# Performance work log

Hardware: AMD Instinct MI355X
Metric: run time of the kernel (lower is better)

## Reference

```python
import jax, jax.numpy as jnp
import numpy as np

N_ENTITY = 64368
N_REL = 40
DIM = 128
NUM_BASES = 8
N_EDGES = 1_200_000
BATCH = 64
MAX_SEED = 32


def setup_inputs() -> dict:
    key = jax.random.key(0)
    ks = jax.random.split(key, 12)
    basis = jax.random.normal(ks[0], (NUM_BASES, N_ENTITY, DIM), jnp.float32) * 0.02
    att = jax.random.normal(ks[1], (N_REL, NUM_BASES), jnp.float32) * 0.1
    root = jax.random.normal(ks[2], (N_ENTITY, DIM), jnp.float32) * 0.02
    rgcn_bias = jnp.zeros((DIM,), jnp.float32)
    xav = 1.414 / np.sqrt(DIM)  # xavier_uniform gain=1.414 scale
    attn_a = jax.random.uniform(ks[3], (DIM, DIM), jnp.float32, -xav, xav)
    attn_b = jax.random.uniform(ks[4], (DIM, 1), jnp.float32, -xav, xav)
    output_bias = jnp.zeros((N_ENTITY,), jnp.float32)
    edge_index = jax.random.randint(ks[5], (2, N_EDGES), 0, N_ENTITY, jnp.int32)
    edge_type = jax.random.randint(ks[6], (N_EDGES,), 0, N_REL, jnp.int32)
    lengths = jax.random.randint(ks[7], (BATCH,), 1, MAX_SEED + 1, jnp.int32)
    seed_mask = jnp.arange(MAX_SEED)[None, :] < lengths[:, None]  # ragged seed sets
    seed_idx = jax.random.randint(ks[8], (BATCH, MAX_SEED), 0, N_ENTITY, jnp.int32)
    labels = jax.random.randint(ks[9], (BATCH,), 0, N_ENTITY, jnp.int32)
    return dict(basis=basis, att=att, root=root, rgcn_bias=rgcn_bias,
                attn_a=attn_a, attn_b=attn_b, output_bias=output_bias,
                edge_index=edge_index, edge_type=edge_type,
                seed_idx=seed_idx, seed_mask=seed_mask, labels=labels)


def reference(basis, att, root, rgcn_bias, attn_a, attn_b, output_bias,
              edge_index, edge_type, seed_idx, seed_mask, labels):
    # ---- RGCNConv with x=None (old PyG): msg_e = (att[rel_e] @ basis)[src_e] ----
    src, dst = edge_index[0], edge_index[1]
    coeff = att[edge_type]                      # [E, B]
    # loop over small fixed num_bases to avoid materializing [B, E, D]
    msg = coeff[:, 0:1] * basis[0][src]         # [E, D]
    for b in range(1, basis.shape[0]):
        msg = msg + coeff[:, b:b + 1] * basis[b][src]
    agg = jax.ops.segment_sum(msg, dst, num_segments=root.shape[0])  # scatter-add
    nodes = agg + root + rgcn_bias              # [N, D] node features

    # ---- per-seed-set gather + self-attention pooling ----
    h = nodes[seed_idx]                         # [Bt, L, D]
    e = jnp.squeeze(jnp.tanh(h @ attn_a) @ attn_b, -1)  # [Bt, L]
    e = jnp.where(seed_mask, e, -jnp.inf)
    attn = jax.nn.softmax(e, axis=-1)
    u = jnp.einsum('bl,bld->bd', attn, h)       # [Bt, D] user reps

    # ---- scores = F.linear(u, nodes, output.bias); CE loss ----
    scores = u @ nodes.T + output_bias          # [Bt, N]
    logp = jax.nn.log_softmax(scores, axis=-1)
    loss = -jnp.mean(jnp.take_along_axis(logp, labels[:, None].astype(jnp.int32), axis=1))
    return scores, loss
```

## Files before the change

kernel.cpp:

```cpp
#include <hip/hip_runtime.h>
#include <hip/hip_bf16.h>

#define N_ENT 64368
#define DIM 128
#define NB 8
#define NREL 40
#define BATCH 64
#define MAXSEED 32
#define OPAD 16

__device__ __forceinline__ unsigned pack_bf2(float x, float y) {
    union { float f; unsigned u; } a, b;
    a.f = x; b.f = y;
    unsigned ra = a.u + 0x7FFFu + ((a.u >> 16) & 1u);
    unsigned rb = b.u + 0x7FFFu + ((b.u >> 16) & 1u);
    return (ra >> 16) | (rb & 0xFFFF0000u);
}

__global__ void mask_norm_kernel(const unsigned char* __restrict__ raw,
                                 int* __restrict__ outMask) {
    __shared__ int s_ni, s_nf;
    int t = threadIdx.x;
    if (t == 0) { s_ni = 0; s_nf = 0; }
    __syncthreads();
    const unsigned int* u32 = (const unsigned int*)raw;
    int not_int = 0, not_flt = 0;
    for (int i = t; i < 512; i += blockDim.x) {
        unsigned int g = u32[i];
        if (g != 0u && g != 1u) not_int = 1;
        if (g != 0u && g != 0x3F800000u) not_flt = 1;
    }
    if (not_int) atomicOr(&s_ni, 1);
    if (not_flt) atomicOr(&s_nf, 1);
    __syncthreads();
    int mode = (!s_ni) ? 0 : ((!s_nf) ? 1 : 2);
    for (int i = t; i < BATCH * MAXSEED; i += blockDim.x) {
        int v;
        if (mode == 0)      v = ((const int*)raw)[i] != 0;
        else if (mode == 1) v = (((const float*)raw)[i] != 0.0f);
        else                v = raw[i] != 0;
        outMask[i] = v;
    }
}

__global__ __launch_bounds__(256) void hist_kernel(
    const int* __restrict__ eidx, int E,
    int* __restrict__ cntS, int* __restrict__ cntD)
{
    const int t = blockIdx.x * blockDim.x + threadIdx.x;
    const int e0 = t * 4;
    if (((E & 3) == 0) && e0 + 3 < E) {
        int4 s4 = *(const int4*)(eidx + e0);
        int4 d4 = *(const int4*)(eidx + E + e0);
        atomicAdd(&cntS[s4.x], 1); atomicAdd(&cntS[s4.y], 1);
        atomicAdd(&cntS[s4.z], 1); atomicAdd(&cntS[s4.w], 1);
        atomicAdd(&cntD[d4.x], 1); atomicAdd(&cntD[d4.y], 1);
        atomicAdd(&cntD[d4.z], 1); atomicAdd(&cntD[d4.w], 1);
    } else {
        for (int e = e0; e < E && e < e0 + 4; ++e) {
            atomicAdd(&cntS[eidx[e]], 1);
            atomicAdd(&cntD[eidx[e + E]], 1);
        }
    }
}

__global__ __launch_bounds__(1024) void scan2_kernel(
    const int* __restrict__ cntS, int* __restrict__ rpS, int* __restrict__ ofS,
    const int* __restrict__ cntD, int* __restrict__ rpD, int* __restrict__ ofD)
{
    const int* cnt = blockIdx.x ? cntD : cntS;
    int* row_ptr   = blockIdx.x ? rpD : rpS;
    int* ofs       = blockIdx.x ? ofD : ofS;
    __shared__ int s[1024];
    const int t = threadIdx.x;
    const int CH = 63;
    const int base = t * CH;
    int sum = 0;
    for (int j = 0; j < CH; ++j) { int p = base + j; if (p < N_ENT) sum += cnt[p]; }
    s[t] = sum;
    for (int off = 1; off < 1024; off <<= 1) {
        __syncthreads();
        int x = (t >= off) ? s[t - off] : 0;
        __syncthreads();
        s[t] += x;
    }
    __syncthreads();
    int run = s[t] - sum;
    for (int j = 0; j < CH; ++j) {
        int p = base + j;
        if (p < N_ENT) { row_ptr[p] = run; ofs[(size_t)p * OPAD] = run; run += cnt[p]; }
    }
    if (t == 1023) row_ptr[N_ENT] = s[1023];
}

__global__ __launch_bounds__(256) void scatS_kernel(
    const int* __restrict__ eidx, const int* __restrict__ etype, int E,
    int* __restrict__ ofsS, unsigned* __restrict__ srcSorted)
{
    const int t = blockIdx.x * blockDim.x + threadIdx.x;
    const int e0 = t * 4;
    if (((E & 3) == 0) && e0 + 3 < E) {
        int4 s4 = *(const int4*)(eidx + e0);
        int4 d4 = *(const int4*)(eidx + E + e0);
        int4 r4 = *(const int4*)(etype + e0);
        int p0 = atomicAdd(&ofsS[(size_t)s4.x * OPAD], 1);
        int p1 = atomicAdd(&ofsS[(size_t)s4.y * OPAD], 1);
        int p2 = atomicAdd(&ofsS[(size_t)s4.z * OPAD], 1);
        int p3 = atomicAdd(&ofsS[(size_t)s4.w * OPAD], 1);
        srcSorted[p0] = ((unsigned)d4.x << 6) | (unsigned)r4.x;
        srcSorted[p1] = ((unsigned)d4.y << 6) | (unsigned)r4.y;
        srcSorted[p2] = ((unsigned)d4.z << 6) | (unsigned)r4.z;
        srcSorted[p3] = ((unsigned)d4.w << 6) | (unsigned)r4.w;
    } else {
        for (int e = e0; e < E && e < e0 + 4; ++e) {
            int p = atomicAdd(&ofsS[(size_t)eidx[e] * OPAD], 1);
            srcSorted[p] = ((unsigned)eidx[e + E] << 6) | (unsigned)etype[e];
        }
    }
}

__global__ __launch_bounds__(256) void msg_kernel(
    const float* __restrict__ basis, const float* __restrict__ att,
    const int* __restrict__ row_ptrS, const unsigned* __restrict__ srcSorted,
    int* __restrict__ ofsD, unsigned* __restrict__ msg)
{
    __shared__ float att_s[NREL * NB];
    const int t = threadIdx.x;
    for (int i = t; i < NREL * NB; i += 256) att_s[i] = att[i];
    __syncthreads();
    const int lane = t & 63;
    const int s = blockIdx.x * 4 + (t >> 6);
    const int r0 = row_ptrS[s], r1 = row_ptrS[s + 1];
    if (r0 == r1) return;
    float2 B[NB];
#pragma unroll
    for (int b = 0; b < NB; ++b)
        B[b] = ((const float2*)(basis + ((size_t)b * N_ENT + s) * DIM))[lane];
    for (int i = r0; i < r1; i += 4) {
        const int m = min(4, r1 - i);
        unsigned pk_l = (lane < m) ? srcSorted[i + lane] : 0u;
        int q_l = 0;
        if (lane < m) q_l = atomicAdd(&ofsD[(size_t)(pk_l >> 6) * OPAD], 1);
        for (int j = 0; j < m; ++j) {
            unsigned pk = (unsigned)__shfl((int)pk_l, j, 64);
            int q = __shfl(q_l, j, 64);
            const float* __restrict__ c = att_s + (pk & 63u) * NB;
            float mx = 0.f, my = 0.f;
#pragma unroll
            for (int b = 0; b < NB; ++b) { mx += c[b] * B[b].x; my += c[b] * B[b].y; }
            __builtin_nontemporal_store(pack_bf2(mx, my), msg + (size_t)q * 64 + lane);
        }
    }
}

__global__ __launch_bounds__(256) void reduce_kernel(
    const unsigned* __restrict__ msg, const int* __restrict__ row_ptrD,
    const float* __restrict__ root, const float* __restrict__ rbias,
    float* __restrict__ nodes)
{
    const int t = threadIdx.x;
    const int lane = t & 63;
    const int d = blockIdx.x * 4 + (t >> 6);
    const int r0 = row_ptrD[d], r1 = row_ptrD[d + 1];
    float2 acc = ((const float2*)(root + (size_t)d * DIM))[lane];
    acc.x += rbias[lane * 2];
    acc.y += rbias[lane * 2 + 1];
    for (int i = r0; i < r1; ++i) {
        unsigned u = __builtin_nontemporal_load(msg + (size_t)i * 64 + lane);
        acc.x += __uint_as_float(u << 16);
        acc.y += __uint_as_float(u & 0xFFFF0000u);
    }
    ((float2*)(nodes + (size_t)d * DIM))[lane] = acc;
}

__global__ __launch_bounds__(256) void edge_atomic_kernel(
    const float* __restrict__ basis, const float* __restrict__ att,
    const int* __restrict__ row_ptrS, const unsigned* __restrict__ srcSorted,
    float* __restrict__ nodes)
{
    __shared__ float att_s[NREL * NB];
    const int t = threadIdx.x;
    for (int i = t; i < NREL * NB; i += 256) att_s[i] = att[i];
    __syncthreads();
    const int lane = t & 63;
    const int s = blockIdx.x * 4 + (t >> 6);
    const int r0 = row_ptrS[s], r1 = row_ptrS[s + 1];
    if (r0 == r1) return;
    float2 B[NB];
#pragma unroll
    for (int b = 0; b < NB; ++b)
        B[b] = ((const float2*)(basis + ((size_t)b * N_ENT + s) * DIM))[lane];
    for (int i = r0; i < r1; ++i) {
        unsigned pk = srcSorted[i];
        const float* __restrict__ c = att_s + (pk & 63u) * NB;
        int d = (int)(pk >> 6);
        float mx = 0.f, my = 0.f;
#pragma unroll
        for (int b = 0; b < NB; ++b) { mx += c[b] * B[b].x; my += c[b] * B[b].y; }
        float* dp = nodes + (size_t)d * DIM + lane * 2;
        unsafeAtomicAdd(dp, mx);
        unsafeAtomicAdd(dp + 1, my);
    }
}

__global__ __launch_bounds__(256) void finalize_nodes(
    float* __restrict__ nodes, const float* __restrict__ root,
    const float* __restrict__ bias, int total)
{
    int i = blockIdx.x * blockDim.x + threadIdx.x;
    if (i < total) nodes[i] = nodes[i] + root[i] + bias[i & (DIM - 1)];
}

__global__ __launch_bounds__(128) void attn_kernel(
    const float* __restrict__ nodes, const float* __restrict__ A,
    const float* __restrict__ bvec, const int* __restrict__ seed_idx,
    const int* __restrict__ maskN, float* __restrict__ u)
{
    __shared__ float A_s[DIM * DIM];
    __shared__ float h_s[MAXSEED * DIM];
    __shared__ float ev[MAXSEED];
    __shared__ float aw[MAXSEED];
    __shared__ float red[2];
    const int b = blockIdx.x;
    const int t = threadIdx.x;

    for (int i = t; i < DIM * DIM; i += 128) A_s[i] = A[i];
    for (int l = 0; l < MAXSEED; ++l) {
        int idx = seed_idx[b * MAXSEED + l];
        h_s[l * DIM + t] = nodes[(size_t)idx * DIM + t];
    }
    __syncthreads();

    const float bv = bvec[t];
    for (int l = 0; l < MAXSEED; ++l) {
        float s = 0.f;
#pragma unroll 8
        for (int d1 = 0; d1 < DIM; ++d1) s += h_s[l * DIM + d1] * A_s[d1 * DIM + t];
        float val = tanhf(s) * bv;
#pragma unroll
        for (int off = 32; off > 0; off >>= 1) val += __shfl_down(val, off, 64);
        if ((t & 63) == 0) red[t >> 6] = val;
        __syncthreads();
        if (t == 0) ev[l] = red[0] + red[1];
        __syncthreads();
    }

    if (t == 0) {
        float mx = -1e30f;
        for (int l = 0; l < MAXSEED; ++l)
            if (maskN[b * MAXSEED + l]) mx = fmaxf(mx, ev[l]);
        float den = 0.f;
        for (int l = 0; l < MAXSEED; ++l) {
            float w = maskN[b * MAXSEED + l] ? expf(ev[l] - mx) : 0.f;
            aw[l] = w;
            den += w;
        }
        float inv = 1.f / den;
        for (int l = 0; l < MAXSEED; ++l) aw[l] *= inv;
    }
    __syncthreads();

    float s = 0.f;
    for (int l = 0; l < MAXSEED; ++l) s += aw[l] * h_s[l * DIM + t];
    u[b * DIM + t] = s;
}

__global__ __launch_bounds__(256) void scores_kernel(
    const float* __restrict__ nodes, const float* __restrict__ u,
    const float* __restrict__ obias, float* __restrict__ out)
{
    __shared__ float u_s[BATCH * DIM];
    const int t = threadIdx.x;
    const int n0 = blockIdx.x * 64;
    for (int i = t; i < BATCH * DIM; i += 256) u_s[i] = u[i];
    __syncthreads();
    const int nl = t & 63, bg = t >> 6;
    const int n = n0 + nl;
    const int nc = n < N_ENT ? n : N_ENT - 1;
    const float4* __restrict__ nrow = (const float4*)(nodes + (size_t)nc * DIM);
    float acc[16];
#pragma unroll
    for (int bi = 0; bi < 16; ++bi) acc[bi] = 0.f;
    for (int dc = 0; dc < DIM / 4; ++dc) {
        const float4 nr = nrow[dc];
#pragma unroll
        for (int bi = 0; bi < 16; ++bi) {
            const float4 uu = *(const float4*)(u_s + (bg * 16 + bi) * DIM + dc * 4);
            acc[bi] += nr.x * uu.x + nr.y * uu.y + nr.z * uu.z + nr.w * uu.w;
        }
    }
    if (n < N_ENT) {
        const float ob = obias[n];
#pragma unroll
        for (int bi = 0; bi < 16; ++bi)
            out[(size_t)(bg * 16 + bi) * N_ENT + n] = acc[bi] + ob;
    }
}

#define LSE_CH 8
__global__ __launch_bounds__(256) void lse1_kernel(
    const float* __restrict__ scores, float2* __restrict__ pls)
{
    const int b = blockIdx.x >> 3, c = blockIdx.x & 7;
    const int t = threadIdx.x;
    const int CH = (N_ENT + LSE_CH - 1) / LSE_CH;
    const int i0 = c * CH, i1 = min(N_ENT, i0 + CH);
    const float* __restrict__ row = scores + (size_t)b * N_ENT;
    __shared__ float red[4], red2[4];
    float mx = -1e30f;
    for (int i = i0 + t; i < i1; i += 256) mx = fmaxf(mx, row[i]);
#pragma unroll
    for (int off = 32; off > 0; off >>= 1) mx = fmaxf(mx, __shfl_down(mx, off, 64));
    if ((t & 63) == 0) red[t >> 6] = mx;
    __syncthreads();
    const float m4 = fmaxf(fmaxf(red[0], red[1]), fmaxf(red[2], red[3]));
    float ss = 0.f;
    for (int i = i0 + t; i < i1; i += 256) ss += expf(row[i] - m4);
#pragma unroll
    for (int off = 32; off > 0; off >>= 1) ss += __shfl_down(ss, off, 64);
    if ((t & 63) == 0) red2[t >> 6] = ss;
    __syncthreads();
    if (t == 0) pls[blockIdx.x] = make_float2(m4, red2[0] + red2[1] + red2[2] + red2[3]);
}

__global__ void lse2_kernel(const float2* __restrict__ pls, float* __restrict__ lse)
{
    const int b = threadIdx.x;
    if (b < BATCH) {
        float M = -1e30f;
        for (int c = 0; c < LSE_CH; ++c) M = fmaxf(M, pls[b * LSE_CH + c].x);
        float S = 0.f;
        for (int c = 0; c < LSE_CH; ++c) {
            float2 p = pls[b * LSE_CH + c];
            S += p.y * expf(p.x - M);
        }
        lse[b] = M + logf(S);
    }
}

__global__ void loss_kernel(const float* __restrict__ scores,
                            const float* __restrict__ lse,
                            const int* __restrict__ labels,
                            float* __restrict__ out_loss)
{
    const int t = threadIdx.x;
    float v = 0.f;
    if (t < BATCH) {
        int lab = labels[t];
        v = lse[t] - scores[(size_t)t * N_ENT + lab];
    }
#pragma unroll
    for (int off = 32; off > 0; off >>= 1) v += __shfl_down(v, off, 64);
    if (t == 0) out_loss[0] = v * (1.0f / BATCH);
}

extern "C" void kernel_launch(void* const* d_in, const int* in_sizes, int n_in,
                              void* d_out, int out_size, void* d_ws, size_t ws_size,
                              hipStream_t stream) {
    const float* basis = (const float*)d_in[0];
    const float* att   = (const float*)d_in[1];
    const float* root  = (const float*)d_in[2];
    const float* rbias = (const float*)d_in[3];
    const float* attnA = (const float*)d_in[4];
    const float* attnB = (const float*)d_in[5];
    const float* obias = (const float*)d_in[6];
    const int* eindex  = (const int*)d_in[7];
    const int* etype   = (const int*)d_in[8];
    const int* sidx    = (const int*)d_in[9];
    const unsigned char* smask = (const unsigned char*)d_in[10];
    const int* labels  = (const int*)d_in[11];
    const int E = in_sizes[8];
    float* out = (float*)d_out;

    auto alignup = [](size_t x) { return (x + 511) & ~(size_t)511; };
    char* p = (char*)d_ws;
    float* nodes = (float*)p;      p += alignup((size_t)N_ENT * DIM * 4);
    float* u     = (float*)p;      p += alignup((size_t)BATCH * DIM * 4);
    float* lse   = (float*)p;      p += alignup(BATCH * 4);
    float2* pls  = (float2*)p;     p += alignup(BATCH * LSE_CH * 8);
    int* maskN   = (int*)p;        p += alignup(BATCH * MAXSEED * 4);
    int* cntS    = (int*)p;
    int* cntD    = cntS + N_ENT;   p += alignup((size_t)2 * N_ENT * 4);
    int* row_ptrS= (int*)p;        p += alignup((size_t)(N_ENT + 1) * 4);
    int* row_ptrD= (int*)p;        p += alignup((size_t)(N_ENT + 1) * 4);
    int* ofsS    = (int*)p;        p += alignup((size_t)N_ENT * OPAD * 4);
    int* ofsD    = (int*)p;        p += alignup((size_t)N_ENT * OPAD * 4);
    unsigned* srcSorted = (unsigned*)p; p += alignup((size_t)E * 4);
    unsigned* msg = (unsigned*)p;  p += alignup((size_t)E * 64 * 4);
    const bool planA = ((size_t)(p - (char*)d_ws) <= ws_size);

    const int gridE4 = ((E + 3) / 4 + 255) / 256;

    mask_norm_kernel<<<1, 256, 0, stream>>>(smask, maskN);
    hipMemsetAsync(cntS, 0, (size_t)2 * N_ENT * 4, stream);
    hist_kernel<<<gridE4, 256, 0, stream>>>(eindex, E, cntS, cntD);
    scan2_kernel<<<2, 1024, 0, stream>>>(cntS, row_ptrS, ofsS, cntD, row_ptrD, ofsD);
    scatS_kernel<<<gridE4, 256, 0, stream>>>(eindex, etype, E, ofsS, srcSorted);

    if (planA) {
        msg_kernel<<<N_ENT / 4, 256, 0, stream>>>(basis, att, row_ptrS, srcSorted, ofsD, msg);
        reduce_kernel<<<N_ENT / 4, 256, 0, stream>>>(msg, row_ptrD, root, rbias, nodes);
    } else {
        hipMemsetAsync(nodes, 0, (size_t)N_ENT * DIM * 4, stream);
        edge_atomic_kernel<<<N_ENT / 4, 256, 0, stream>>>(basis, att, row_ptrS, srcSorted, nodes);
        finalize_nodes<<<((N_ENT * DIM) + 255) / 256, 256, 0, stream>>>(nodes, root, rbias, N_ENT * DIM);
    }

    attn_kernel<<<BATCH, 128, 0, stream>>>(nodes, attnA, attnB, sidx, maskN, u);
    scores_kernel<<<(N_ENT + 63) / 64, 256, 0, stream>>>(nodes, u, obias, out);
    lse1_kernel<<<BATCH * LSE_CH, 256, 0, stream>>>(out, pls);
    lse2_kernel<<<1, 64, 0, stream>>>(pls, lse);
    loss_kernel<<<1, 64, 0, stream>>>(out, lse, labels, out + (size_t)BATCH * N_ENT);
}
```

Measured before the change: 1.041 ms.

## Store edge messages as scaled FP8, fuse LSE into scores, fold mask into attention

Edge messages are now stored as scaled FP8 pairs instead of BF16 when the compiler offers the pack/unpack builtins, halving the E×128 message buffer traffic between msg_kernel and reduce_kernel. The reduce loop is unrolled by four with independent accumulators. Per-block partial max and sum-exp are computed inside scores_kernel, which removes the separate pass that reread the 64×N score matrix. Mask normalisation moves into attn_kernel, dropping one launch. FP8 with a fixed scale of 128 loses a lot of message precision and may push results past tolerance.

```diff
diff --git a/kernel.cpp b/kernel.cpp
--- a/kernel.cpp
+++ b/kernel.cpp
@@ -8,6 +8,21 @@
 #define BATCH 64
 #define MAXSEED 32
 #define OPAD 16
+#define NBLK ((N_ENT + 63) / 64)
+
+#if defined(__has_builtin)
+#if __has_builtin(__builtin_amdgcn_cvt_pk_fp8_f32) && __has_builtin(__builtin_amdgcn_cvt_pk_f32_fp8)
+#define USE_FP8 1
+#endif
+#endif
+#ifndef USE_FP8
+#define USE_FP8 0
+#endif
+
+#define MSG_SCALE 128.0f
+#define MSG_INV_SCALE (1.0f / 128.0f)
+
+typedef float v2f __attribute__((ext_vector_type(2)));
 
 __device__ __forceinline__ unsigned pack_bf2(float x, float y) {
     union { float f; unsigned u; } a, b;
@@ -15,32 +30,6 @@
     unsigned ra = a.u + 0x7FFFu + ((a.u >> 16) & 1u);
     unsigned rb = b.u + 0x7FFFu + ((b.u >> 16) & 1u);
     return (ra >> 16) | (rb & 0xFFFF0000u);
-}
-
-__global__ void mask_norm_kernel(const unsigned char* __restrict__ raw,
-                                 int* __restrict__ outMask) {
-    __shared__ int s_ni, s_nf;
-    int t = threadIdx.x;
-    if (t == 0) { s_ni = 0; s_nf = 0; }
-    __syncthreads();
-    const unsigned int* u32 = (const unsigned int*)raw;
-    int not_int = 0, not_flt = 0;
-    for (int i = t; i < 512; i += blockDim.x) {
-        unsigned int g = u32[i];
-        if (g != 0u && g != 1u) not_int = 1;
-        if (g != 0u && g != 0x3F800000u) not_flt = 1;
-    }
-    if (not_int) atomicOr(&s_ni, 1);
-    if (not_flt) atomicOr(&s_nf, 1);
-    __syncthreads();
-    int mode = (!s_ni) ? 0 : ((!s_nf) ? 1 : 2);
-    for (int i = t; i < BATCH * MAXSEED; i += blockDim.x) {
-        int v;
-        if (mode == 0)      v = ((const int*)raw)[i] != 0;
-        else if (mode == 1) v = (((const float*)raw)[i] != 0.0f);
-        else                v = raw[i] != 0;
-        outMask[i] = v;
-    }
 }
 
 __global__ __launch_bounds__(256) void hist_kernel(
@@ -122,11 +111,12 @@
 __global__ __launch_bounds__(256) void msg_kernel(
     const float* __restrict__ basis, const float* __restrict__ att,
     const int* __restrict__ row_ptrS, const unsigned* __restrict__ srcSorted,
-    int* __restrict__ ofsD, unsigned* __restrict__ msg)
+    int* __restrict__ ofsD, void* __restrict__ msgv)
 {
     __shared__ float att_s[NREL * NB];
     const int t = threadIdx.x;
-    for (int i = t; i < NREL * NB; i += 256) att_s[i] = att[i];
+    const float ascale = USE_FP8 ? MSG_SCALE : 1.0f;
+    for (int i = t; i < NREL * NB; i += 256) att_s[i] = att[i] * ascale;
     __syncthreads();
     const int lane = t & 63;
     const int s = blockIdx.x * 4 + (t >> 6);
@@ -136,6 +126,11 @@
 #pragma unroll
     for (int b = 0; b < NB; ++b)
         B[b] = ((const float2*)(basis + ((size_t)b * N_ENT + s) * DIM))[lane];
+#if USE_FP8
+    unsigned short* __restrict__ msg8 = (unsigned short*)msgv;
+#else
+    unsigned* __restrict__ msg = (unsigned*)msgv;
+#endif
     for (int i = r0; i < r1; i += 4) {
         const int m = min(4, r1 - i);
         unsigned pk_l = (lane < m) ? srcSorted[i + lane] : 0u;
@@ -148,13 +143,20 @@
             float mx = 0.f, my = 0.f;
 #pragma unroll
             for (int b = 0; b < NB; ++b) { mx += c[b] * B[b].x; my += c[b] * B[b].y; }
-            __builtin_nontemporal_store(pack_bf2(mx, my), msg + (size_t)q * 64 + lane);
+#if USE_FP8
+            int p8 = __builtin_amdgcn_cvt_pk_fp8_f32(mx, my, 0, false);
+            __builtin_nontemporal_store((unsigned short)p8,
+                                        msg8 + (size_t)q * 64 + lane);
+#else
+            __builtin_nontemporal_store(pack_bf2(mx, my),
+                                        (unsigned*)msg + (size_t)q * 64 + lane);
+#endif
         }
     }
 }
 
 __global__ __launch_bounds__(256) void reduce_kernel(
-    const unsigned* __restrict__ msg, const int* __restrict__ row_ptrD,
+    const void* __restrict__ msgv, const int* __restrict__ row_ptrD,
     const float* __restrict__ root, const float* __restrict__ rbias,
     float* __restrict__ nodes)
 {
@@ -162,14 +164,49 @@
     const int lane = t & 63;
     const int d = blockIdx.x * 4 + (t >> 6);
     const int r0 = row_ptrD[d], r1 = row_ptrD[d + 1];
+    float ax0 = 0.f, ay0 = 0.f, ax1 = 0.f, ay1 = 0.f;
+    float ax2 = 0.f, ay2 = 0.f, ax3 = 0.f, ay3 = 0.f;
+    int i = r0;
+#if USE_FP8
+    const unsigned short* __restrict__ msg8 = (const unsigned short*)msgv;
+    for (; i + 3 < r1; i += 4) {
+        unsigned short v0 = __builtin_nontemporal_load(msg8 + (size_t)(i + 0) * 64 + lane);
+        unsigned short v1 = __builtin_nontemporal_load(msg8 + (size_t)(i + 1) * 64 + lane);
+        unsigned short v2 = __builtin_nontemporal_load(msg8 + (size_t)(i + 2) * 64 + lane);
+        unsigned short v3 = __builtin_nontemporal_load(msg8 + (size_t)(i + 3) * 64 + lane);
+        v2f f0 = __builtin_amdgcn_cvt_pk_f32_fp8((int)v0, false);
+        v2f f1 = __builtin_amdgcn_cvt_pk_f32_fp8((int)v1, false);
+        v2f f2 = __builtin_amdgcn_cvt_pk_f32_fp8((int)v2, false);
+        v2f f3 = __builtin_amdgcn_cvt_pk_f32_fp8((int)v3, false);
+        ax0 += f0.x; ay0 += f0.y; ax1 += f1.x; ay1 += f1.y;
+        ax2 += f2.x; ay2 += f2.y; ax3 += f3.x; ay3 += f3.y;
+    }
+    for (; i < r1; ++i) {
+        unsigned short v = __builtin_nontemporal_load(msg8 + (size_t)i * 64 + lane);
+        v2f f = __builtin_amdgcn_cvt_pk_f32_fp8((int)v, false);
+        ax0 += f.x; ay0 += f.y;
+    }
+#else
+    const unsigned* __restrict__ msg = (const unsigned*)msgv;
+    for (; i + 3 < r1; i += 4) {
+        unsigned u0 = __builtin_nontemporal_load(msg + (size_t)(i + 0) * 64 + lane);
+        unsigned u1 = __builtin_nontemporal_load(msg + (size_t)(i + 1) * 64 + lane);
+        unsigned u2 = __builtin_nontemporal_load(msg + (size_t)(i + 2) * 64 + lane);
+        unsigned u3 = __builtin_nontemporal_load(msg + (size_t)(i + 3) * 64 + lane);
+        ax0 += __uint_as_float(u0 << 16); ay0 += __uint_as_float(u0 & 0xFFFF0000u);
+        ax1 += __uint_as_float(u1 << 16); ay1 += __uint_as_float(u1 & 0xFFFF0000u);
+        ax2 += __uint_as_float(u2 << 16); ay2 += __uint_as_float(u2 & 0xFFFF0000u);
+        ax3 += __uint_as_float(u3 << 16); ay3 += __uint_as_float(u3 & 0xFFFF0000u);
+    }
+    for (; i < r1; ++i) {
+        unsigned u = __builtin_nontemporal_load(msg + (size_t)i * 64 + lane);
+        ax0 += __uint_as_float(u << 16); ay0 += __uint_as_float(u & 0xFFFF0000u);
+    }
+#endif
+    const float unscale = USE_FP8 ? MSG_INV_SCALE : 1.0f;
     float2 acc = ((const float2*)(root + (size_t)d * DIM))[lane];
-    acc.x += rbias[lane * 2];
-    acc.y += rbias[lane * 2 + 1];
-    for (int i = r0; i < r1; ++i) {
-        unsigned u = __builtin_nontemporal_load(msg + (size_t)i * 64 + lane);
-        acc.x += __uint_as_float(u << 16);
-        acc.y += __uint_as_float(u & 0xFFFF0000u);
-    }
+    acc.x += rbias[lane * 2]     + ((ax0 + ax1) + (ax2 + ax3)) * unscale;
+    acc.y += rbias[lane * 2 + 1] + ((ay0 + ay1) + (ay2 + ay3)) * unscale;
     ((float2*)(nodes + (size_t)d * DIM))[lane] = acc;
 }
 
@@ -214,20 +251,46 @@
 __global__ __launch_bounds__(128) void attn_kernel(
     const float* __restrict__ nodes, const float* __restrict__ A,
     const float* __restrict__ bvec, const int* __restrict__ seed_idx,
-    const int* __restrict__ maskN, float* __restrict__ u)
+    const unsigned char* __restrict__ rawmask, float* __restrict__ u)
 {
     __shared__ float A_s[DIM * DIM];
     __shared__ float h_s[MAXSEED * DIM];
     __shared__ float ev[MAXSEED];
     __shared__ float aw[MAXSEED];
     __shared__ float red[2];
+    __shared__ int m_s[MAXSEED];
+    __shared__ int s_ni, s_nf;
     const int b = blockIdx.x;
     const int t = threadIdx.x;
+
+    if (t == 0) { s_ni = 0; s_nf = 0; }
+    __syncthreads();
+    {
+        const unsigned int* u32 = (const unsigned int*)rawmask;
+        int not_int = 0, not_flt = 0;
+        for (int i = t; i < 512; i += 128) {
+            unsigned g = u32[i];
+            if (g != 0u && g != 1u) not_int = 1;
+            if (g != 0u && g != 0x3F800000u) not_flt = 1;
+        }
+        if (not_int) atomicOr(&s_ni, 1);
+        if (not_flt) atomicOr(&s_nf, 1);
+    }
 
     for (int i = t; i < DIM * DIM; i += 128) A_s[i] = A[i];
     for (int l = 0; l < MAXSEED; ++l) {
         int idx = seed_idx[b * MAXSEED + l];
         h_s[l * DIM + t] = nodes[(size_t)idx * DIM + t];
+    }
+    __syncthreads();
+    if (t < MAXSEED) {
+        int mode = (!s_ni) ? 0 : ((!s_nf) ? 1 : 2);
+        int gi = b * MAXSEED + t;
+        int v;
+        if (mode == 0)      v = ((const int*)rawmask)[gi] != 0;
+        else if (mode == 1) v = (((const float*)rawmask)[gi] != 0.0f);
+        else                v = rawmask[gi] != 0;
+        m_s[t] = v;
     }
     __syncthreads();
 
@@ -248,10 +311,10 @@
     if (t == 0) {
         float mx = -1e30f;
         for (int l = 0; l < MAXSEED; ++l)
-            if (maskN[b * MAXSEED + l]) mx = fmaxf(mx, ev[l]);
+            if (m_s[l]) mx = fmaxf(mx, ev[l]);
         float den = 0.f;
         for (int l = 0; l < MAXSEED; ++l) {
-            float w = maskN[b * MAXSEED + l] ? expf(ev[l] - mx) : 0.f;
+            float w = m_s[l] ? expf(ev[l] - mx) : 0.f;
             aw[l] = w;
             den += w;
         }
@@ -267,7 +330,8 @@
 
 __global__ __launch_bounds__(256) void scores_kernel(
     const float* __restrict__ nodes, const float* __restrict__ u,
-    const float* __restrict__ obias, float* __restrict__ out)
+    const float* __restrict__ obias, float* __restrict__ out,
+    float2* __restrict__ pls)
 {
     __shared__ float u_s[BATCH * DIM];
     const int t = threadIdx.x;
@@ -276,7 +340,8 @@
     __syncthreads();
     const int nl = t & 63, bg = t >> 6;
     const int n = n0 + nl;
-    const int nc = n < N_ENT ? n : N_ENT - 1;
+    const bool valid = (n < N_ENT);
+    const int nc = valid ? n : N_ENT - 1;
     const float4* __restrict__ nrow = (const float4*)(nodes + (size_t)nc * DIM);
     float acc[16];
 #pragma unroll
@@ -289,53 +354,45 @@
             acc[bi] += nr.x * uu.x + nr.y * uu.y + nr.z * uu.z + nr.w * uu.w;
         }
     }
-    if (n < N_ENT) {
-        const float ob = obias[n];
-#pragma unroll
-        for (int bi = 0; bi < 16; ++bi)
-            out[(size_t)(bg * 16 + bi) * N_ENT + n] = acc[bi] + ob;
-    }
-}
-
-#define LSE_CH 8
-__global__ __launch_bounds__(256) void lse1_kernel(
-    const float* __restrict__ scores, float2* __restrict__ pls)
-{
-    const int b = blockIdx.x >> 3, c = blockIdx.x & 7;
-    const int t = threadIdx.x;
-    const int CH = (N_ENT + LSE_CH - 1) / LSE_CH;
-    const int i0 = c * CH, i1 = min(N_ENT, i0 + CH);
-    const float* __restrict__ row = scores + (size_t)b * N_ENT;
+    const float ob = valid ? obias[n] : 0.f;
+#pragma unroll
+    for (int bi = 0; bi < 16; ++bi) {
+        float v = valid ? acc[bi] + ob : -INFINITY;
+        if (valid) out[(size_t)(bg * 16 + bi) * N_ENT + n] = v;
+        float m = v;
+#pragma unroll
+        for (int mk = 1; mk < 64; mk <<= 1) m = fmaxf(m, __shfl_xor(m, mk, 64));
+        float e = valid ? __expf(v - m) : 0.f;
+#pragma unroll
+        for (int mk = 1; mk < 64; mk <<= 1) e += __shfl_xor(e, mk, 64);
+        if (nl == 0)
+            pls[(size_t)(bg * 16 + bi) * NBLK + blockIdx.x] = make_float2(m, e);
+    }
+}
+
+__global__ __launch_bounds__(256) void lse2_kernel(
+    const float2* __restrict__ pls, float* __restrict__ lse)
+{
     __shared__ float red[4], red2[4];
+    const int b = blockIdx.x, t = threadIdx.x;
+    const float2* __restrict__ row = pls + (size_t)b * NBLK;
     float mx = -1e30f;
-    for (int i = i0 + t; i < i1; i += 256) mx = fmaxf(mx, row[i]);
+    for (int i = t; i < NBLK; i += 256) mx = fmaxf(mx, row[i].x);
 #pragma unroll
     for (int off = 32; off > 0; off >>= 1) mx = fmaxf(mx, __shfl_down(mx, off, 64));
     if ((t & 63) == 0) red[t >> 6] = mx;
     __syncthreads();
-    const float m4 = fmaxf(fmaxf(red[0], red[1]), fmaxf(red[2], red[3]));
-    float ss = 0.f;
-    for (int i = i0 + t; i < i1; i += 256) ss += expf(row[i] - m4);
-#pragma unroll
-    for (int off = 32; off > 0; off >>= 1) ss += __shfl_down(ss, off, 64);
-    if ((t & 63) == 0) red2[t >> 6] = ss;
-    __syncthreads();
-    if (t == 0) pls[blockIdx.x] = make_float2(m4, red2[0] + red2[1] + red2[2] + red2[3]);
-}
-
-__global__ void lse2_kernel(const float2* __restrict__ pls, float* __restrict__ lse)
-{
-    const int b = threadIdx.x;
-    if (b < BATCH) {
-        float M = -1e30f;
-        for (int c = 0; c < LSE_CH; ++c) M = fmaxf(M, pls[b * LSE_CH + c].x);
-        float S = 0.f;
-        for (int c = 0; c < LSE_CH; ++c) {
-            float2 p = pls[b * LSE_CH + c];
-            S += p.y * expf(p.x - M);
-        }
-        lse[b] = M + logf(S);
-    }
+    const float M = fmaxf(fmaxf(red[0], red[1]), fmaxf(red[2], red[3]));
+    float s = 0.f;
+    for (int i = t; i < NBLK; i += 256) {
+        float2 p = row[i];
+        s += p.y * expf(p.x - M);
+    }
+#pragma unroll
+    for (int off = 32; off > 0; off >>= 1) s += __shfl_down(s, off, 64);
+    if ((t & 63) == 0) red2[t >> 6] = s;
+    __syncthreads();
+    if (t == 0) lse[b] = M + logf(red2[0] + red2[1] + red2[2] + red2[3]);
 }
 
 __global__ void loss_kernel(const float* __restrict__ scores,
@@ -377,8 +434,7 @@
     float* nodes = (float*)p;      p += alignup((size_t)N_ENT * DIM * 4);
     float* u     = (float*)p;      p += alignup((size_t)BATCH * DIM * 4);
     float* lse   = (float*)p;      p += alignup(BATCH * 4);
-    float2* pls  = (float2*)p;     p += alignup(BATCH * LSE_CH * 8);
-    int* maskN   = (int*)p;        p += alignup(BATCH * MAXSEED * 4);
+    float2* pls  = (float2*)p;     p += alignup((size_t)BATCH * NBLK * 8);
     int* cntS    = (int*)p;
     int* cntD    = cntS + N_ENT;   p += alignup((size_t)2 * N_ENT * 4);
     int* row_ptrS= (int*)p;        p += alignup((size_t)(N_ENT + 1) * 4);
@@ -386,12 +442,11 @@
     int* ofsS    = (int*)p;        p += alignup((size_t)N_ENT * OPAD * 4);
     int* ofsD    = (int*)p;        p += alignup((size_t)N_ENT * OPAD * 4);
     unsigned* srcSorted = (unsigned*)p; p += alignup((size_t)E * 4);
-    unsigned* msg = (unsigned*)p;  p += alignup((size_t)E * 64 * 4);
+    void* msg    = (void*)p;       p += alignup((size_t)E * 64 * 4);
     const bool planA = ((size_t)(p - (char*)d_ws) <= ws_size);
 
     const int gridE4 = ((E + 3) / 4 + 255) / 256;
 
-    mask_norm_kernel<<<1, 256, 0, stream>>>(smask, maskN);
     hipMemsetAsync(cntS, 0, (size_t)2 * N_ENT * 4, stream);
     hist_kernel<<<gridE4, 256, 0, stream>>>(eindex, E, cntS, cntD);
     scan2_kernel<<<2, 1024, 0, stream>>>(cntS, row_ptrS, ofsS, cntD, row_ptrD, ofsD);
@@ -406,9 +461,8 @@
         finalize_nodes<<<((N_ENT * DIM) + 255) / 256, 256, 0, stream>>>(nodes, root, rbias, N_ENT * DIM);
     }
 
-    attn_kernel<<<BATCH, 128, 0, stream>>>(nodes, attnA, attnB, sidx, maskN, u);
-    scores_kernel<<<(N_ENT + 63) / 64, 256, 0, stream>>>(nodes, u, obias, out);
-    lse1_kernel<<<BATCH * LSE_CH, 256, 0, stream>>>(out, pls);
-    lse2_kernel<<<1, 64, 0, stream>>>(pls, lse);
+    attn_kernel<<<BATCH, 128, 0, stream>>>(nodes, attnA, attnB, sidx, smask, u);
+    scores_kernel<<<NBLK, 256, 0, stream>>>(nodes, u, obias, out, pls);
+    lse2_kernel<<<BATCH, 256, 0, stream>>>(pls, lse);
     loss_kernel<<<1, 64, 0, stream>>>(out, lse, labels, out + (size_t)BATCH * N_ENT);
 }
```

Measured after the change: 968.1 us. 7.0% less time.
